# Kernel optimization log

Hardware: AMD Instinct MI355X
Metric: run time of the kernel (lower is better)

Reference implementation:

```python
import jax, jax.numpy as jnp
import numpy as np

N = 100000
D = 64
H = 4 * D  # 256
E = 1000000


def setup_inputs() -> dict:
    key = jax.random.key(0)
    ks = jax.random.split(key, 9)
    return {
        "loc_feat": jax.random.normal(ks[0], (N, D), dtype=jnp.float32),
        "geo_src": jax.random.randint(ks[1], (E,), 0, N),
        "geo_dst": jax.random.randint(ks[2], (E,), 0, N),
        "trans_src": jax.random.randint(ks[3], (E,), 0, N),
        "trans_dst": jax.random.randint(ks[4], (E,), 0, N),
        "trans_w": jax.random.uniform(ks[5], (E,), dtype=jnp.float32),
        "W1": jax.random.normal(ks[6], (D, H), dtype=jnp.float32) * (1.0 / np.sqrt(D)),
        "b1": jax.random.normal(ks[7], (H,), dtype=jnp.float32) * 0.01,
        "W2": jax.random.normal(ks[8], (H, 1), dtype=jnp.float32) * (1.0 / np.sqrt(H)),
    }


def reference(loc_feat, geo_src, geo_dst, trans_src, trans_dst, trans_w, W1, b1, W2):
    n = loc_feat.shape[0]
    # etype 'geo': copy_u + mean  -> segment mean of src features at dst
    geo_sum = jax.ops.segment_sum(loc_feat[geo_src], geo_dst, num_segments=n)
    cnt = jax.ops.segment_sum(jnp.ones(geo_src.shape[0], loc_feat.dtype), geo_dst, num_segments=n)
    geo = jnp.where(cnt[:, None] > 0, geo_sum / jnp.maximum(cnt, 1.0)[:, None], 0.0)
    # etype 'trans': u_mul_e + sum -> weighted segment sum
    trans = jax.ops.segment_sum(loc_feat[trans_src] * trans_w[:, None], trans_dst, num_segments=n)
    # semantic attention fuse over the two relation views
    z = jnp.stack([geo, trans], axis=1)          # [N, 2, D]
    h = jnp.tanh(jnp.einsum('nkd,dh->nkh', z, W1) + b1)  # [N, 2, H]
    w = jnp.einsum('nkh,ho->nko', h, W2).mean(0)  # [2, 1] (mean over nodes)
    beta = jax.nn.softmax(w, axis=0)              # [2, 1]
    return (beta[None, :, :] * z).sum(1)          # [N, D]
```

## Files before the change

kernel.cpp:

```cpp
#include <hip/hip_runtime.h>
#include <hip/hip_bf16.h>

#define N_NODES 100000
#define DIM 64
#define HID 256
#define E_EDGES 1000000
#define TWO_N (2 * N_NODES)
#define MLP_ROWBLOCKS (TWO_N / 64)

#define TILE 120
#define NBINS 834
#define CAP 1600
#define EPB 4096
#define FILL_BLOCKS 245

typedef short short8 __attribute__((ext_vector_type(8)));
typedef float f32x4 __attribute__((ext_vector_type(4)));
typedef unsigned short us4 __attribute__((ext_vector_type(4)));

__device__ __forceinline__ float tanh_fast(float x) {
    x = fminf(fmaxf(x, -15.0f), 15.0f);
    float e = __expf(2.0f * x);
    return (e - 1.0f) / (e + 1.0f);
}

__device__ __forceinline__ unsigned short f2bf(float x) {
    unsigned u = __float_as_uint(x);
    u = u + 0x7FFFu + ((u >> 16) & 1u);
    return (unsigned short)(u >> 16);
}

__device__ __forceinline__ float bf2f(unsigned short u) {
    return __uint_as_float(((unsigned)u) << 16);
}

__global__ void pack_feat_kernel(const float* __restrict__ feat,
                                 unsigned short* __restrict__ fb) {
    int i = blockIdx.x * 256 + threadIdx.x;
    float4 v = ((const float4*)feat)[i];
    us4 o;
    o[0] = f2bf(v.x); o[1] = f2bf(v.y); o[2] = f2bf(v.z); o[3] = f2bf(v.w);
    ((us4*)fb)[i] = o;
}

__global__ void __launch_bounds__(512) bin_fill_kernel(
        const int* __restrict__ gs, const int* __restrict__ gd,
        const int* __restrict__ ts, const int* __restrict__ td,
        const float* __restrict__ tw,
        int* __restrict__ gcount,
        int* __restrict__ gbin, int2* __restrict__ tbin) {
    __shared__ int   hist[NBINS];
    __shared__ int   adjS[NBINS];
    __shared__ int   curS[NBINS];
    __shared__ int   pS[EPB];
    __shared__ float w2S[EPB];
    __shared__ unsigned short binS[EPB];
    __shared__ int   scanS[512];

    int t = threadIdx.x;
    int blk = blockIdx.x;
    int rel = (blk >= FILL_BLOCKS) ? 1 : 0;
    int e0 = (rel ? blk - FILL_BLOCKS : blk) * EPB;
    const int* dstp = rel ? td : gd;
    const int* srcp = rel ? ts : gs;

    for (int i = t; i < NBINS; i += 512) hist[i] = 0;
    __syncthreads();

    int d_[8], s_[8];
    float w_[8];
    #pragma unroll
    for (int j = 0; j < 2; ++j) {
        int idx = e0 + j * 2048 + 4 * t;
        if (idx + 3 < E_EDGES) {
            int4 dv = *(const int4*)&dstp[idx];
            int4 sv = *(const int4*)&srcp[idx];
            d_[4*j+0] = dv.x; d_[4*j+1] = dv.y; d_[4*j+2] = dv.z; d_[4*j+3] = dv.w;
            s_[4*j+0] = sv.x; s_[4*j+1] = sv.y; s_[4*j+2] = sv.z; s_[4*j+3] = sv.w;
            if (rel) {
                float4 wv = *(const float4*)&tw[idx];
                w_[4*j+0] = wv.x; w_[4*j+1] = wv.y; w_[4*j+2] = wv.z; w_[4*j+3] = wv.w;
            }
        } else {
            #pragma unroll
            for (int i2 = 0; i2 < 4; ++i2) {
                bool ok = (idx + i2 < E_EDGES);
                d_[4*j+i2] = ok ? dstp[idx + i2] : -1;
                s_[4*j+i2] = ok ? srcp[idx + i2] : 0;
                w_[4*j+i2] = (ok && rel) ? tw[idx + i2] : 0.0f;
            }
        }
    }
    #pragma unroll
    for (int i = 0; i < 8; ++i)
        if (d_[i] >= 0) atomicAdd(&hist[d_[i] / TILE], 1);
    __syncthreads();

    int carry = 0;
    for (int cb = 0; cb < NBINS; cb += 512) {
        int i = cb + t;
        int c = (i < NBINS) ? hist[i] : 0;
        __syncthreads();
        scanS[t] = c;
        __syncthreads();
        int v = c;
        #pragma unroll
        for (int off = 1; off < 512; off <<= 1) {
            int add = (t >= off) ? scanS[t - off] : 0;
            __syncthreads();
            v += add;
            scanS[t] = v;
            __syncthreads();
        }
        if (i < NBINS) {
            int lb = v - c + carry;
            curS[i] = lb;
            int gb = (c > 0) ? (i * CAP + atomicAdd(&gcount[rel * NBINS + i], c)) : 0;
            adjS[i] = gb - lb;
        }
        carry += scanS[511];
    }
    __syncthreads();

    #pragma unroll
    for (int i = 0; i < 8; ++i) {
        int d = d_[i];
        if (d < 0) continue;
        int bin = d / TILE;
        int pos = atomicAdd(&curS[bin], 1);
        pS[pos] = s_[i] | ((d - bin * TILE) << 20);
        binS[pos] = (unsigned short)bin;
        if (rel) w2S[pos] = w_[i];
    }
    __syncthreads();

    int nV = min(EPB, E_EDGES - e0);
    if (!rel) {
        for (int i = t; i < nV; i += 512) {
            int b = binS[i];
            int gi = adjS[b] + i;
            if (gi < (b + 1) * CAP)
                gbin[gi] = pS[i];
        }
    } else {
        for (int i = t; i < nV; i += 512) {
            int b = binS[i];
            int gi = adjS[b] + i;
            if (gi < (b + 1) * CAP)
                tbin[gi] = make_int2(pS[i], __float_as_int(w2S[i]));
        }
    }
}

__global__ void __launch_bounds__(256) aggregate_kernel(
        const unsigned short* __restrict__ featb,
        const int* __restrict__ gbin, const int2* __restrict__ tbin,
        const int* __restrict__ gcount,
        unsigned short* __restrict__ zb) {
    __shared__ int   srcS[CAP];
    __shared__ float wS[CAP];
    __shared__ int   histS[TILE];
    __shared__ int   baseS[TILE];
    __shared__ int   curS[TILE];
    __shared__ int   scanS[128];

    int b = blockIdx.x;
    int rel = (b >= NBINS) ? 1 : 0;
    int bin = rel ? b - NBINS : b;
    int node0 = bin * TILE;
    int nNodes = min(TILE, N_NODES - node0);
    int t = threadIdx.x, lane = t & 63, wave = t >> 6;
    int q = lane >> 4, ql = lane & 15;

    int nE = gcount[b];
    if (nE > CAP) nE = CAP;

    for (int i = t; i < TILE; i += 256) histS[i] = 0;
    __syncthreads();

    if (!rel) {
        const int* bp = gbin + (size_t)bin * CAP;
        for (int i = t; i < nE; i += 256) atomicAdd(&histS[bp[i] >> 20], 1);
    } else {
        const int2* bp = tbin + (size_t)bin * CAP;
        for (int i = t; i < nE; i += 256) atomicAdd(&histS[bp[i].x >> 20], 1);
    }
    __syncthreads();

    if (t < 128) scanS[t] = (t < TILE) ? histS[t] : 0;
    __syncthreads();
    #pragma unroll
    for (int off = 1; off < 128; off <<= 1) {
        int add = 0;
        if (t < 128 && t >= off) add = scanS[t - off];
        __syncthreads();
        if (t < 128) scanS[t] += add;
        __syncthreads();
    }
    if (t < TILE) {
        int base = scanS[t] - histS[t];
        baseS[t] = base;
        curS[t] = base;
    }
    __syncthreads();

    if (!rel) {
        const int* bp = gbin + (size_t)bin * CAP;
        for (int i = t; i < nE; i += 256) {
            int p = bp[i];
            int pos = atomicAdd(&curS[p >> 20], 1);
            srcS[pos] = p & 0xFFFFF;
        }
    } else {
        const int2* bp = tbin + (size_t)bin * CAP;
        for (int i = t; i < nE; i += 256) {
            int2 p = bp[i];
            int pos = atomicAdd(&curS[p.x >> 20], 1);
            srcS[pos] = p.x & 0xFFFFF;
            wS[pos] = __int_as_float(p.y);
        }
    }
    __syncthreads();

    for (int nl0 = wave * 4; nl0 < nNodes; nl0 += 16) {
        int nl = nl0 + q;
        bool act = (nl < nNodes);
        int deg = act ? histS[nl] : 0;
        int base = act ? baseS[nl] : 0;
        float a0 = 0.f, a1 = 0.f, a2 = 0.f, a3 = 0.f;
        if (!rel) {
            int k = 0;
            for (; k + 3 < deg; k += 4) {
                int s0 = srcS[base + k], s1 = srcS[base + k + 1];
                int s2 = srcS[base + k + 2], s3 = srcS[base + k + 3];
                us4 r0 = *(const us4*)&featb[(size_t)s0 * DIM + ql * 4];
                us4 r1 = *(const us4*)&featb[(size_t)s1 * DIM + ql * 4];
                us4 r2 = *(const us4*)&featb[(size_t)s2 * DIM + ql * 4];
                us4 r3 = *(const us4*)&featb[(size_t)s3 * DIM + ql * 4];
                a0 += (bf2f(r0[0]) + bf2f(r1[0])) + (bf2f(r2[0]) + bf2f(r3[0]));
                a1 += (bf2f(r0[1]) + bf2f(r1[1])) + (bf2f(r2[1]) + bf2f(r3[1]));
                a2 += (bf2f(r0[2]) + bf2f(r1[2])) + (bf2f(r2[2]) + bf2f(r3[2]));
                a3 += (bf2f(r0[3]) + bf2f(r1[3])) + (bf2f(r2[3]) + bf2f(r3[3]));
            }
            for (; k < deg; ++k) {
                int s = srcS[base + k];
                us4 r = *(const us4*)&featb[(size_t)s * DIM + ql * 4];
                a0 += bf2f(r[0]); a1 += bf2f(r[1]);
                a2 += bf2f(r[2]); a3 += bf2f(r[3]);
            }
        } else {
            int k = 0;
            for (; k + 3 < deg; k += 4) {
                int s0 = srcS[base + k], s1 = srcS[base + k + 1];
                int s2 = srcS[base + k + 2], s3 = srcS[base + k + 3];
                float w0 = wS[base + k], w1 = wS[base + k + 1];
                float w2 = wS[base + k + 2], w3 = wS[base + k + 3];
                us4 r0 = *(const us4*)&featb[(size_t)s0 * DIM + ql * 4];
                us4 r1 = *(const us4*)&featb[(size_t)s1 * DIM + ql * 4];
                us4 r2 = *(const us4*)&featb[(size_t)s2 * DIM + ql * 4];
                us4 r3 = *(const us4*)&featb[(size_t)s3 * DIM + ql * 4];
                a0 += (bf2f(r0[0]) * w0 + bf2f(r1[0]) * w1) + (bf2f(r2[0]) * w2 + bf2f(r3[0]) * w3);
                a1 += (bf2f(r0[1]) * w0 + bf2f(r1[1]) * w1) + (bf2f(r2[1]) * w2 + bf2f(r3[1]) * w3);
                a2 += (bf2f(r0[2]) * w0 + bf2f(r1[2]) * w1) + (bf2f(r2[2]) * w2 + bf2f(r3[2]) * w3);
                a3 += (bf2f(r0[3]) * w0 + bf2f(r1[3]) * w1) + (bf2f(r2[3]) * w2 + bf2f(r3[3]) * w3);
            }
            for (; k < deg; ++k) {
                int s = srcS[base + k];
                float w = wS[base + k];
                us4 r = *(const us4*)&featb[(size_t)s * DIM + ql * 4];
                a0 += bf2f(r[0]) * w; a1 += bf2f(r[1]) * w;
                a2 += bf2f(r[2]) * w; a3 += bf2f(r[3]) * w;
            }
        }
        if (act) {
            float sc = rel ? 1.0f : 1.0f / fmaxf((float)deg, 1.0f);
            us4 o;
            o[0] = f2bf(a0 * sc); o[1] = f2bf(a1 * sc);
            o[2] = f2bf(a2 * sc); o[3] = f2bf(a3 * sc);
            size_t row = (size_t)(rel ? N_NODES + node0 + nl : node0 + nl);
            *(us4*)&zb[row * DIM + ql * 4] = o;
        }
    }
}

__global__ void pack_w1_kernel(const float* __restrict__ W1, unsigned short* __restrict__ W1p) {
    int i = blockIdx.x * 256 + threadIdx.x;
    int j = i & 7;
    int r = i >> 3;
    int nidx = r & 15; r >>= 4;
    int q = r & 3; r >>= 2;
    int khalf = r & 1;
    int n = r >> 1;
    int k = 32 * khalf + 8 * q + j;
    int c = 16 * n + nidx;
    W1p[i] = f2bf(W1[k * HID + c]);
}

__global__ void __launch_bounds__(256) mlp_mfma_kernel(
        const unsigned short* __restrict__ zb,
        const unsigned short* __restrict__ W1p,
        const float* __restrict__ bias1, const float* __restrict__ W2,
        float* __restrict__ partials) {
    __shared__ float wred[4][2];
    int t = threadIdx.x, lane = t & 63, wave = t >> 6;
    int m = lane & 15, q = lane >> 4;
    int base = blockIdx.x * 64 + wave * 16;
    int R = base + m;

    const unsigned short* rowp = zb + (size_t)R * DIM;
    short8 a0 = *(const short8*)(rowp + q * 8);
    short8 a1 = *(const short8*)(rowp + 32 + q * 8);

    float c0 = 0.0f, c1 = 0.0f;
    const short8* W1v = (const short8*)W1p;

    #pragma unroll 4
    for (int n = 0; n < 16; ++n) {
        short8 b0 = W1v[(n * 2 + 0) * 64 + lane];
        short8 bK = W1v[(n * 2 + 1) * 64 + lane];
        f32x4 acc = {0.0f, 0.0f, 0.0f, 0.0f};
        acc = __builtin_amdgcn_mfma_f32_16x16x32_bf16(a0, b0, acc, 0, 0, 0);
        acc = __builtin_amdgcn_mfma_f32_16x16x32_bf16(a1, bK, acc, 0, 0, 0);
        int col = 16 * n + m;
        float bj = bias1[col];
        float w2 = W2[col];
        #pragma unroll
        for (int reg = 0; reg < 4; ++reg) {
            int Rr = base + q * 4 + reg;
            float h = tanh_fast(acc[reg] + bj);
            float contrib = h * w2;
            if (Rr < N_NODES) c0 += contrib; else c1 += contrib;
        }
    }

    #pragma unroll
    for (int off = 32; off > 0; off >>= 1) {
        c0 += __shfl_down(c0, off);
        c1 += __shfl_down(c1, off);
    }
    if (lane == 0) { wred[wave][0] = c0; wred[wave][1] = c1; }
    __syncthreads();
    if (t == 0) {
        partials[blockIdx.x * 2 + 0] = wred[0][0] + wred[1][0] + wred[2][0] + wred[3][0];
        partials[blockIdx.x * 2 + 1] = wred[0][1] + wred[1][1] + wred[2][1] + wred[3][1];
    }
}

__global__ void beta_kernel(const float* __restrict__ partials, float* __restrict__ beta) {
    __shared__ float wred[4][2];
    int t = threadIdx.x;
    float c0 = 0.0f, c1 = 0.0f;
    for (int i = t; i < MLP_ROWBLOCKS; i += 256) {
        c0 += partials[i * 2 + 0];
        c1 += partials[i * 2 + 1];
    }
    #pragma unroll
    for (int off = 32; off > 0; off >>= 1) {
        c0 += __shfl_down(c0, off);
        c1 += __shfl_down(c1, off);
    }
    int lane = t & 63, wv = t >> 6;
    if (lane == 0) { wred[wv][0] = c0; wred[wv][1] = c1; }
    __syncthreads();
    if (t == 0) {
        float s0 = (wred[0][0] + wred[1][0] + wred[2][0] + wred[3][0]) / (float)N_NODES;
        float s1 = (wred[0][1] + wred[1][1] + wred[2][1] + wred[3][1]) / (float)N_NODES;
        float m = fmaxf(s0, s1);
        float e0 = __expf(s0 - m), e1 = __expf(s1 - m);
        float inv = 1.0f / (e0 + e1);
        beta[0] = e0 * inv;
        beta[1] = e1 * inv;
    }
}

__global__ void combine_kernel(const unsigned short* __restrict__ zb,
                               const float* __restrict__ beta,
                               float* __restrict__ out) {
    int gid = blockIdx.x * 256 + threadIdx.x;
    float b0 = beta[0];
    float b1 = beta[1];
    uint4 g = *(const uint4*)&zb[(size_t)gid * 8];
    uint4 tr = *(const uint4*)&zb[(size_t)N_NODES * DIM + (size_t)gid * 8];
    float4 o0, o1;
    o0.x = b0 * __uint_as_float(g.x << 16) + b1 * __uint_as_float(tr.x << 16);
    o0.y = b0 * __uint_as_float(g.x & 0xFFFF0000u) + b1 * __uint_as_float(tr.x & 0xFFFF0000u);
    o0.z = b0 * __uint_as_float(g.y << 16) + b1 * __uint_as_float(tr.y << 16);
    o0.w = b0 * __uint_as_float(g.y & 0xFFFF0000u) + b1 * __uint_as_float(tr.y & 0xFFFF0000u);
    o1.x = b0 * __uint_as_float(g.z << 16) + b1 * __uint_as_float(tr.z << 16);
    o1.y = b0 * __uint_as_float(g.z & 0xFFFF0000u) + b1 * __uint_as_float(tr.z & 0xFFFF0000u);
    o1.z = b0 * __uint_as_float(g.w << 16) + b1 * __uint_as_float(tr.w << 16);
    o1.w = b0 * __uint_as_float(g.w & 0xFFFF0000u) + b1 * __uint_as_float(tr.w & 0xFFFF0000u);
    *(float4*)&out[(size_t)gid * 8] = o0;
    *(float4*)&out[(size_t)gid * 8 + 4] = o1;
}

extern "C" void kernel_launch(void* const* d_in, const int* in_sizes, int n_in,
                              void* d_out, int out_size, void* d_ws, size_t ws_size,
                              hipStream_t stream) {
    const float* loc_feat = (const float*)d_in[0];
    const int* geo_src    = (const int*)d_in[1];
    const int* geo_dst    = (const int*)d_in[2];
    const int* trans_src  = (const int*)d_in[3];
    const int* trans_dst  = (const int*)d_in[4];
    const float* trans_w  = (const float*)d_in[5];
    const float* W1       = (const float*)d_in[6];
    const float* b1       = (const float*)d_in[7];
    const float* W2       = (const float*)d_in[8];
    float* out = (float*)d_out;

    int*   gcount   = (int*)d_ws;
    int*   gbin     = gcount + 2 * NBINS;
    int2*  tbin     = (int2*)(gbin + (size_t)NBINS * CAP);
    float* partials = (float*)(tbin + (size_t)NBINS * CAP);
    float* beta     = partials + 2 * MLP_ROWBLOCKS;
    unsigned short* W1p   = (unsigned short*)(beta + 2);
    unsigned short* featb = W1p + 16384;
    unsigned short* zb    = featb + (size_t)N_NODES * DIM;

    hipMemsetAsync(gcount, 0, 2 * NBINS * sizeof(int), stream);

    pack_feat_kernel<<<(N_NODES * DIM / 4) / 256, 256, 0, stream>>>(loc_feat, featb);
    pack_w1_kernel<<<64, 256, 0, stream>>>(W1, W1p);
    bin_fill_kernel<<<2 * FILL_BLOCKS, 512, 0, stream>>>(geo_src, geo_dst, trans_src,
                                                         trans_dst, trans_w,
                                                         gcount, gbin, tbin);
    aggregate_kernel<<<2 * NBINS, 256, 0, stream>>>(featb, gbin, tbin, gcount, zb);
    mlp_mfma_kernel<<<MLP_ROWBLOCKS, 256, 0, stream>>>(zb, W1p, b1, W2, partials);
    beta_kernel<<<1, 256, 0, stream>>>(partials, beta);
    combine_kernel<<<(N_NODES * DIM / 8) / 256, 256, 0, stream>>>(zb, beta, out);
}
```

Before: 233.9 us.

## Use wave-shuffle scans, merge pack kernels, and unroll gather loops by eight

Replaces the shared-memory Hillis-Steele scans in bin_fill and aggregate with wave-level __shfl_up scans plus a small cross-wave fixup, removing many __syncthreads barriers. Merges the feature and W1 packing kernels into one launch, with a single extra block packing W1 serially. Unrolls the gather-accumulate loops from four to eight neighbours to keep more loads in flight. This trades more register pressure and a slower single-block W1 pack for fewer barriers and launches.

```diff
diff --git a/kernel.cpp b/kernel.cpp
--- a/kernel.cpp
+++ b/kernel.cpp
@@ -13,6 +13,7 @@
 #define CAP 1600
 #define EPB 4096
 #define FILL_BLOCKS 245
+#define FEAT_BLOCKS ((N_NODES * DIM / 4) / 256)
 
 typedef short short8 __attribute__((ext_vector_type(8)));
 typedef float f32x4 __attribute__((ext_vector_type(4)));
@@ -34,13 +35,28 @@
     return __uint_as_float(((unsigned)u) << 16);
 }
 
-__global__ void pack_feat_kernel(const float* __restrict__ feat,
-                                 unsigned short* __restrict__ fb) {
-    int i = blockIdx.x * 256 + threadIdx.x;
-    float4 v = ((const float4*)feat)[i];
-    us4 o;
-    o[0] = f2bf(v.x); o[1] = f2bf(v.y); o[2] = f2bf(v.z); o[3] = f2bf(v.w);
-    ((us4*)fb)[i] = o;
+__global__ void pack_kernel(const float* __restrict__ feat, unsigned short* __restrict__ fb,
+                            const float* __restrict__ W1, unsigned short* __restrict__ W1p) {
+    int b = blockIdx.x;
+    if (b < FEAT_BLOCKS) {
+        int i = b * 256 + threadIdx.x;
+        float4 v = ((const float4*)feat)[i];
+        us4 o;
+        o[0] = f2bf(v.x); o[1] = f2bf(v.y); o[2] = f2bf(v.z); o[3] = f2bf(v.w);
+        ((us4*)fb)[i] = o;
+    } else {
+        for (int i = threadIdx.x; i < 16384; i += 256) {
+            int j = i & 7;
+            int r = i >> 3;
+            int nidx = r & 15; r >>= 4;
+            int q = r & 3; r >>= 2;
+            int khalf = r & 1;
+            int n = r >> 1;
+            int k = 32 * khalf + 8 * q + j;
+            int c = 16 * n + nidx;
+            W1p[i] = f2bf(W1[k * HID + c]);
+        }
+    }
 }
 
 __global__ void __launch_bounds__(512) bin_fill_kernel(
@@ -55,9 +71,9 @@
     __shared__ int   pS[EPB];
     __shared__ float w2S[EPB];
     __shared__ unsigned short binS[EPB];
-    __shared__ int   scanS[512];
-
-    int t = threadIdx.x;
+    __shared__ int   wsumS[8];
+
+    int t = threadIdx.x, lane = t & 63, wid = t >> 6;
     int blk = blockIdx.x;
     int rel = (blk >= FILL_BLOCKS) ? 1 : 0;
     int e0 = (rel ? blk - FILL_BLOCKS : blk) * EPB;
@@ -96,29 +112,35 @@
         if (d_[i] >= 0) atomicAdd(&hist[d_[i] / TILE], 1);
     __syncthreads();
 
-    int carry = 0;
-    for (int cb = 0; cb < NBINS; cb += 512) {
-        int i = cb + t;
-        int c = (i < NBINS) ? hist[i] : 0;
-        __syncthreads();
-        scanS[t] = c;
-        __syncthreads();
-        int v = c;
+    int b0i = 2 * t, b1i = 2 * t + 1;
+    int h0 = (b0i < NBINS) ? hist[b0i] : 0;
+    int h1 = (b1i < NBINS) ? hist[b1i] : 0;
+    int c = h0 + h1;
+    int v = c;
+    #pragma unroll
+    for (int off = 1; off < 64; off <<= 1) {
+        int u = __shfl_up(v, off);
+        if (lane >= off) v += u;
+    }
+    if (lane == 63) wsumS[wid] = v;
+    __syncthreads();
+    if (t == 0) {
+        int run = 0;
         #pragma unroll
-        for (int off = 1; off < 512; off <<= 1) {
-            int add = (t >= off) ? scanS[t - off] : 0;
-            __syncthreads();
-            v += add;
-            scanS[t] = v;
-            __syncthreads();
-        }
-        if (i < NBINS) {
-            int lb = v - c + carry;
-            curS[i] = lb;
-            int gb = (c > 0) ? (i * CAP + atomicAdd(&gcount[rel * NBINS + i], c)) : 0;
-            adjS[i] = gb - lb;
-        }
-        carry += scanS[511];
+        for (int i = 0; i < 8; ++i) { int x = wsumS[i]; wsumS[i] = run; run += x; }
+    }
+    __syncthreads();
+    int excl = v - c + wsumS[wid];
+    if (b0i < NBINS) {
+        curS[b0i] = excl;
+        int gb = (h0 > 0) ? (b0i * CAP + atomicAdd(&gcount[rel * NBINS + b0i], h0)) : 0;
+        adjS[b0i] = gb - excl;
+    }
+    if (b1i < NBINS) {
+        int lb1 = excl + h0;
+        curS[b1i] = lb1;
+        int gb = (h1 > 0) ? (b1i * CAP + atomicAdd(&gcount[rel * NBINS + b1i], h1)) : 0;
+        adjS[b1i] = gb - lb1;
     }
     __syncthreads();
 
@@ -162,7 +184,7 @@
     __shared__ int   histS[TILE];
     __shared__ int   baseS[TILE];
     __shared__ int   curS[TILE];
-    __shared__ int   scanS[128];
+    __shared__ int   w0sum[1];
 
     int b = blockIdx.x;
     int rel = (b >= NBINS) ? 1 : 0;
@@ -187,18 +209,18 @@
     }
     __syncthreads();
 
-    if (t < 128) scanS[t] = (t < TILE) ? histS[t] : 0;
-    __syncthreads();
-    #pragma unroll
-    for (int off = 1; off < 128; off <<= 1) {
-        int add = 0;
-        if (t < 128 && t >= off) add = scanS[t - off];
-        __syncthreads();
-        if (t < 128) scanS[t] += add;
-        __syncthreads();
-    }
+    int h = (t < TILE) ? histS[t] : 0;
+    int v = h;
+    #pragma unroll
+    for (int off = 1; off < 64; off <<= 1) {
+        int u = __shfl_up(v, off);
+        if (lane >= off) v += u;
+    }
+    if (t == 63) w0sum[0] = v;
+    __syncthreads();
+    if (wave == 1) v += w0sum[0];
     if (t < TILE) {
-        int base = scanS[t] - histS[t];
+        int base = v - h;
         baseS[t] = base;
         curS[t] = base;
     }
@@ -230,19 +252,38 @@
         float a0 = 0.f, a1 = 0.f, a2 = 0.f, a3 = 0.f;
         if (!rel) {
             int k = 0;
-            for (; k + 3 < deg; k += 4) {
-                int s0 = srcS[base + k], s1 = srcS[base + k + 1];
+            for (; k + 7 < deg; k += 8) {
+                int s0 = srcS[base + k],     s1 = srcS[base + k + 1];
                 int s2 = srcS[base + k + 2], s3 = srcS[base + k + 3];
+                int s4 = srcS[base + k + 4], s5 = srcS[base + k + 5];
+                int s6 = srcS[base + k + 6], s7 = srcS[base + k + 7];
                 us4 r0 = *(const us4*)&featb[(size_t)s0 * DIM + ql * 4];
                 us4 r1 = *(const us4*)&featb[(size_t)s1 * DIM + ql * 4];
                 us4 r2 = *(const us4*)&featb[(size_t)s2 * DIM + ql * 4];
                 us4 r3 = *(const us4*)&featb[(size_t)s3 * DIM + ql * 4];
-                a0 += (bf2f(r0[0]) + bf2f(r1[0])) + (bf2f(r2[0]) + bf2f(r3[0]));
-                a1 += (bf2f(r0[1]) + bf2f(r1[1])) + (bf2f(r2[1]) + bf2f(r3[1]));
-                a2 += (bf2f(r0[2]) + bf2f(r1[2])) + (bf2f(r2[2]) + bf2f(r3[2]));
-                a3 += (bf2f(r0[3]) + bf2f(r1[3])) + (bf2f(r2[3]) + bf2f(r3[3]));
-            }
-            for (; k < deg; ++k) {
+                us4 r4 = *(const us4*)&featb[(size_t)s4 * DIM + ql * 4];
+                us4 r5 = *(const us4*)&featb[(size_t)s5 * DIM + ql * 4];
+                us4 r6 = *(const us4*)&featb[(size_t)s6 * DIM + ql * 4];
+                us4 r7 = *(const us4*)&featb[(size_t)s7 * DIM + ql * 4];
+                a0 += ((bf2f(r0[0]) + bf2f(r1[0])) + (bf2f(r2[0]) + bf2f(r3[0])))
+                    + ((bf2f(r4[0]) + bf2f(r5[0])) + (bf2f(r6[0]) + bf2f(r7[0])));
+                a1 += ((bf2f(r0[1]) + bf2f(r1[1])) + (bf2f(r2[1]) + bf2f(r3[1])))
+                    + ((bf2f(r4[1]) + bf2f(r5[1])) + (bf2f(r6[1]) + bf2f(r7[1])));
+                a2 += ((bf2f(r0[2]) + bf2f(r1[2])) + (bf2f(r2[2]) + bf2f(r3[2])))
+                    + ((bf2f(r4[2]) + bf2f(r5[2])) + (bf2f(r6[2]) + bf2f(r7[2])));
+                a3 += ((bf2f(r0[3]) + bf2f(r1[3])) + (bf2f(r2[3]) + bf2f(r3[3])))
+                    + ((bf2f(r4[3]) + bf2f(r5[3])) + (bf2f(r6[3]) + bf2f(r7[3])));
+            }
+            for (; k + 1 < deg; k += 2) {
+                int s0 = srcS[base + k], s1 = srcS[base + k + 1];
+                us4 r0 = *(const us4*)&featb[(size_t)s0 * DIM + ql * 4];
+                us4 r1 = *(const us4*)&featb[(size_t)s1 * DIM + ql * 4];
+                a0 += bf2f(r0[0]) + bf2f(r1[0]);
+                a1 += bf2f(r0[1]) + bf2f(r1[1]);
+                a2 += bf2f(r0[2]) + bf2f(r1[2]);
+                a3 += bf2f(r0[3]) + bf2f(r1[3]);
+            }
+            if (k < deg) {
                 int s = srcS[base + k];
                 us4 r = *(const us4*)&featb[(size_t)s * DIM + ql * 4];
                 a0 += bf2f(r[0]); a1 += bf2f(r[1]);
@@ -250,21 +291,43 @@
             }
         } else {
             int k = 0;
-            for (; k + 3 < deg; k += 4) {
-                int s0 = srcS[base + k], s1 = srcS[base + k + 1];
+            for (; k + 7 < deg; k += 8) {
+                int s0 = srcS[base + k],     s1 = srcS[base + k + 1];
                 int s2 = srcS[base + k + 2], s3 = srcS[base + k + 3];
-                float w0 = wS[base + k], w1 = wS[base + k + 1];
+                int s4 = srcS[base + k + 4], s5 = srcS[base + k + 5];
+                int s6 = srcS[base + k + 6], s7 = srcS[base + k + 7];
+                float w0 = wS[base + k],     w1 = wS[base + k + 1];
                 float w2 = wS[base + k + 2], w3 = wS[base + k + 3];
+                float w4 = wS[base + k + 4], w5 = wS[base + k + 5];
+                float w6 = wS[base + k + 6], w7 = wS[base + k + 7];
                 us4 r0 = *(const us4*)&featb[(size_t)s0 * DIM + ql * 4];
                 us4 r1 = *(const us4*)&featb[(size_t)s1 * DIM + ql * 4];
                 us4 r2 = *(const us4*)&featb[(size_t)s2 * DIM + ql * 4];
                 us4 r3 = *(const us4*)&featb[(size_t)s3 * DIM + ql * 4];
-                a0 += (bf2f(r0[0]) * w0 + bf2f(r1[0]) * w1) + (bf2f(r2[0]) * w2 + bf2f(r3[0]) * w3);
-                a1 += (bf2f(r0[1]) * w0 + bf2f(r1[1]) * w1) + (bf2f(r2[1]) * w2 + bf2f(r3[1]) * w3);
-                a2 += (bf2f(r0[2]) * w0 + bf2f(r1[2]) * w1) + (bf2f(r2[2]) * w2 + bf2f(r3[2]) * w3);
-                a3 += (bf2f(r0[3]) * w0 + bf2f(r1[3]) * w1) + (bf2f(r2[3]) * w2 + bf2f(r3[3]) * w3);
-            }
-            for (; k < deg; ++k) {
+                us4 r4 = *(const us4*)&featb[(size_t)s4 * DIM + ql * 4];
+                us4 r5 = *(const us4*)&featb[(size_t)s5 * DIM + ql * 4];
+                us4 r6 = *(const us4*)&featb[(size_t)s6 * DIM + ql * 4];
+                us4 r7 = *(const us4*)&featb[(size_t)s7 * DIM + ql * 4];
+                a0 += ((bf2f(r0[0])*w0 + bf2f(r1[0])*w1) + (bf2f(r2[0])*w2 + bf2f(r3[0])*w3))
+                    + ((bf2f(r4[0])*w4 + bf2f(r5[0])*w5) + (bf2f(r6[0])*w6 + bf2f(r7[0])*w7));
+                a1 += ((bf2f(r0[1])*w0 + bf2f(r1[1])*w1) + (bf2f(r2[1])*w2 + bf2f(r3[1])*w3))
+                    + ((bf2f(r4[1])*w4 + bf2f(r5[1])*w5) + (bf2f(r6[1])*w6 + bf2f(r7[1])*w7));
+                a2 += ((bf2f(r0[2])*w0 + bf2f(r1[2])*w1) + (bf2f(r2[2])*w2 + bf2f(r3[2])*w3))
+                    + ((bf2f(r4[2])*w4 + bf2f(r5[2])*w5) + (bf2f(r6[2])*w6 + bf2f(r7[2])*w7));
+                a3 += ((bf2f(r0[3])*w0 + bf2f(r1[3])*w1) + (bf2f(r2[3])*w2 + bf2f(r3[3])*w3))
+                    + ((bf2f(r4[3])*w4 + bf2f(r5[3])*w5) + (bf2f(r6[3])*w6 + bf2f(r7[3])*w7));
+            }
+            for (; k + 1 < deg; k += 2) {
+                int s0 = srcS[base + k], s1 = srcS[base + k + 1];
+                float w0 = wS[base + k], w1 = wS[base + k + 1];
+                us4 r0 = *(const us4*)&featb[(size_t)s0 * DIM + ql * 4];
+                us4 r1 = *(const us4*)&featb[(size_t)s1 * DIM + ql * 4];
+                a0 += bf2f(r0[0]) * w0 + bf2f(r1[0]) * w1;
+                a1 += bf2f(r0[1]) * w0 + bf2f(r1[1]) * w1;
+                a2 += bf2f(r0[2]) * w0 + bf2f(r1[2]) * w1;
+                a3 += bf2f(r0[3]) * w0 + bf2f(r1[3]) * w1;
+            }
+            if (k < deg) {
                 int s = srcS[base + k];
                 float w = wS[base + k];
                 us4 r = *(const us4*)&featb[(size_t)s * DIM + ql * 4];
@@ -281,19 +344,6 @@
             *(us4*)&zb[row * DIM + ql * 4] = o;
         }
     }
-}
-
-__global__ void pack_w1_kernel(const float* __restrict__ W1, unsigned short* __restrict__ W1p) {
-    int i = blockIdx.x * 256 + threadIdx.x;
-    int j = i & 7;
-    int r = i >> 3;
-    int nidx = r & 15; r >>= 4;
-    int q = r & 3; r >>= 2;
-    int khalf = r & 1;
-    int n = r >> 1;
-    int k = 32 * khalf + 8 * q + j;
-    int c = 16 * n + nidx;
-    W1p[i] = f2bf(W1[k * HID + c]);
 }
 
 __global__ void __launch_bounds__(256) mlp_mfma_kernel(
@@ -419,8 +469,7 @@
 
     hipMemsetAsync(gcount, 0, 2 * NBINS * sizeof(int), stream);
 
-    pack_feat_kernel<<<(N_NODES * DIM / 4) / 256, 256, 0, stream>>>(loc_feat, featb);
-    pack_w1_kernel<<<64, 256, 0, stream>>>(W1, W1p);
+    pack_kernel<<<FEAT_BLOCKS + 1, 256, 0, stream>>>(loc_feat, featb, W1, W1p);
     bin_fill_kernel<<<2 * FILL_BLOCKS, 512, 0, stream>>>(geo_src, geo_dst, trans_src,
                                                          trans_dst, trans_w,
                                                          gcount, gbin, tbin);
```

Measured after the change: 246.2 us. 5.3% more time.
